# Performance work log

Measured on AMD Instinct MI355X. Metric: run time of the kernel, lower is better.

Reference implementation:

```python
import jax, jax.numpy as jnp
import numpy as np

EMBED = 768
NH = 12          # num_heads
NL = 3           # num_levels
NP = 4           # num_points
DV = 384         # value dim = embed_dim * deform_ratio(0.5)
DH = DV // NH    # per-head value dim = 32
B = 16
LQ = 1024        # (512/16)^2 ViT tokens
SHAPES = [(64, 64), (32, 32), (16, 16)]  # 1/8, 1/16, 1/32 pyramid of 512x512
LKV = sum(h * w for h, w in SHAPES)      # 5376
EPS = 1e-6


def layer_norm(x, w, b):
    mu = jnp.mean(x, axis=-1, keepdims=True)
    var = jnp.mean((x - mu) ** 2, axis=-1, keepdims=True)
    return (x - mu) / jnp.sqrt(var + EPS) * w + b


def bilinear_sample(v, loc, H, W):
    # v: (B, NH, H*W, DH); loc: (B, Lq, NH, P, 2) normalized in [0,1]
    # Matches torch grid_sample(align_corners=False, padding_mode='zeros').
    Bv, Lq = loc.shape[0], loc.shape[1]
    x = loc[..., 0] * W - 0.5
    y = loc[..., 1] * H - 0.5
    x0 = jnp.floor(x)
    y0 = jnp.floor(y)
    dx = x - x0
    dy = y - y0
    x0i = x0.astype(jnp.int32)
    y0i = y0.astype(jnp.int32)

    def gather(xi, yi):
        valid = (xi >= 0) & (xi < W) & (yi >= 0) & (yi < H)  # (B,Lq,NH,P)
        xc = jnp.clip(xi, 0, W - 1)
        yc = jnp.clip(yi, 0, H - 1)
        lin = (yc * W + xc).transpose(0, 2, 1, 3).reshape(Bv, NH, Lq * NP)
        g = jnp.take_along_axis(v, lin[..., None], axis=2)  # (B,NH,Lq*P,DH)
        g = g.reshape(Bv, NH, Lq, NP, DH).transpose(0, 2, 1, 3, 4)  # (B,Lq,NH,P,DH)
        return g * valid[..., None].astype(g.dtype)

    g00 = gather(x0i, y0i)
    g01 = gather(x0i + 1, y0i)
    g10 = gather(x0i, y0i + 1)
    g11 = gather(x0i + 1, y0i + 1)
    w00 = ((1 - dx) * (1 - dy))[..., None]
    w01 = (dx * (1 - dy))[..., None]
    w10 = ((1 - dx) * dy)[..., None]
    w11 = (dx * dy)[..., None]
    return g00 * w00 + g01 * w01 + g10 * w10 + g11 * w11


def ms_deform_attn_core(value, shapes_list, loc, aw):
    # value: (B,LKV,NH,DH); loc: (B,Lq,NH,NL,NP,2); aw: (B,Lq,NH,NL,NP)
    Bv, Lq = loc.shape[0], loc.shape[1]
    samples = []
    idx = 0
    for l, (H, W) in enumerate(shapes_list):
        v = value[:, idx:idx + H * W].transpose(0, 2, 1, 3)  # (B,NH,HW,DH)
        idx += H * W
        samples.append(bilinear_sample(v, loc[:, :, :, l], H, W))
    s = jnp.stack(samples, axis=3)  # (B,Lq,NH,NL,NP,DH)
    o = jnp.einsum('bqhlp,bqhlpd->bqhd', aw, s)
    return o.reshape(Bv, Lq, NH * DH)


def setup_inputs() -> dict:
    key = jax.random.key(0)
    ks = jax.random.split(key, 12)

    def n(k, shape, s=0.02):
        return jax.random.normal(k, shape, jnp.float32) * s

    return {
        'q': jax.random.normal(ks[0], (B, LQ, EMBED), jnp.float32),
        'reference_points': jax.random.uniform(ks[1], (B, LQ, NL, 2), jnp.float32),
        'kv': jax.random.normal(ks[2], (B, LKV, EMBED), jnp.float32),
        'spatial_shapes': jnp.asarray(SHAPES, jnp.int32),
        'level_start_index': jnp.asarray(
            np.cumsum([0] + [h * w for h, w in SHAPES])[:-1], jnp.int32),
        'ln1_w': jnp.ones(EMBED, jnp.float32),
        'ln1_b': jnp.zeros(EMBED, jnp.float32),
        'ln2_w': jnp.ones(EMBED, jnp.float32),
        'ln2_b': jnp.zeros(EMBED, jnp.float32),
        'gamma': n(ks[3], (EMBED,), 0.1),
        'w_off': n(ks[4], (EMBED, NH * NL * NP * 2)),
        'b_off': n(ks[5], (NH * NL * NP * 2,), 0.01),
        'w_aw': n(ks[6], (EMBED, NH * NL * NP)),
        'b_aw': jnp.zeros(NH * NL * NP, jnp.float32),
        'w_val': n(ks[7], (EMBED, DV)),
        'b_val': jnp.zeros(DV, jnp.float32),
        'w_out': n(ks[8], (DV, EMBED)),
        'b_out': jnp.zeros(EMBED, jnp.float32),
    }


def reference(q, reference_points, kv, spatial_shapes, level_start_index,
              ln1_w, ln1_b, ln2_w, ln2_b, gamma,
              w_off, b_off, w_aw, b_aw, w_val, b_val, w_out, b_out):
    shapes_list = [tuple(int(v) for v in r) for r in np.asarray(spatial_shapes)]
    Bq, Lq, _ = q.shape
    qn = layer_norm(q, ln1_w, ln1_b)
    kvn = layer_norm(kv, ln2_w, ln2_b)
    value = (kvn @ w_val + b_val).reshape(Bq, -1, NH, DH)
    off = (qn @ w_off + b_off).reshape(Bq, Lq, NH, NL, NP, 2)
    aw = (qn @ w_aw + b_aw).reshape(Bq, Lq, NH, NL * NP)
    aw = jax.nn.softmax(aw, axis=-1).reshape(Bq, Lq, NH, NL, NP)
    # offset normalizer is (W_l, H_l) per level
    wh = jnp.asarray([[w, h] for (h, w) in shapes_list], q.dtype)  # (NL,2)
    loc = reference_points[:, :, None, :, None, :] + off / wh[None, None, None, :, None, :]
    attn = ms_deform_attn_core(value, shapes_list, loc, aw)
    attn = attn @ w_out + b_out
    return q + gamma * attn
```

## Files before the change

kernel.cpp:

```cpp
#include <hip/hip_runtime.h>

#define DEV __device__ __forceinline__

typedef short bf16x8 __attribute__((ext_vector_type(8)));
typedef float f32x4 __attribute__((ext_vector_type(4)));

DEV short f2bf(float f) {
  union { float f; unsigned u; } un; un.f = f;
  unsigned r = un.u + 0x7FFFu + ((un.u >> 16) & 1u);
  return (short)(r >> 16);
}
DEV float bf2f(unsigned short s) {
  union { unsigned u; float f; } un;
  un.u = ((unsigned)s) << 16;
  return un.f;
}

DEV float blockReduceSum256(float v, volatile float* sbuf) {
  #pragma unroll
  for (int off = 32; off > 0; off >>= 1) v += __shfl_down(v, off, 64);
  const int wv = threadIdx.x >> 6, ln = threadIdx.x & 63;
  if (ln == 0) sbuf[wv] = v;
  __syncthreads();
  return sbuf[0] + sbuf[1] + sbuf[2] + sbuf[3];
}

__global__ __launch_bounds__(256) void pack_weights_kernel(
    const float* __restrict__ w_val, const float* __restrict__ w_off,
    const float* __restrict__ w_aw, const float* __restrict__ w_out,
    const float* __restrict__ b_off, const float* __restrict__ b_aw,
    short* __restrict__ wT_val, short* __restrict__ wT_offaw,
    short* __restrict__ wT_out, float* __restrict__ bias_cat) {
  int gid = blockIdx.x * 256 + threadIdx.x;
  const int S0 = 768 * 384, S1 = 768 * 288, S2 = 768 * 144, S3 = 384 * 768;
  const int S4 = 16 * 768, S5 = 448;
  if (gid < S0) { int k = gid / 384, n = gid % 384; wT_val[n * 768 + k] = f2bf(w_val[gid]); return; }
  gid -= S0;
  if (gid < S1) { int k = gid / 288, n = gid % 288; wT_offaw[n * 768 + k] = f2bf(w_off[gid]); return; }
  gid -= S1;
  if (gid < S2) { int k = gid / 144, n = gid % 144; wT_offaw[(288 + n) * 768 + k] = f2bf(w_aw[gid]); return; }
  gid -= S2;
  if (gid < S3) { int k = gid / 768, n = gid % 768; wT_out[n * 384 + k] = f2bf(w_out[gid]); return; }
  gid -= S3;
  if (gid < S4) { wT_offaw[432 * 768 + gid] = 0; return; }
  gid -= S4;
  if (gid < S5) { bias_cat[gid] = (gid < 288) ? b_off[gid] : (gid < 432 ? b_aw[gid - 288] : 0.f); }
}

__global__ __launch_bounds__(256) void ln_stats_kernel(const float* __restrict__ x,
                                                       float2* __restrict__ st) {
  const int row = blockIdx.x;
  const float* xr = x + (size_t)row * 768;
  const int t = threadIdx.x;
  float a0 = xr[t], a1 = xr[t + 256], a2 = xr[t + 512];
  __shared__ float sb1[4], sb2[4];
  float mu = blockReduceSum256(a0 + a1 + a2, sb1) * (1.f / 768.f);
  float d0 = a0 - mu, d1 = a1 - mu, d2 = a2 - mu;
  float var = blockReduceSum256(d0 * d0 + d1 * d1 + d2 * d2, sb2) * (1.f / 768.f);
  if (t == 0) st[row] = make_float2(mu, rsqrtf(var + 1e-6f));
}

template <int NT2, int AMODE, int EMODE>
__global__ __launch_bounds__(256, 2) void gemmw_kernel(
    const short* __restrict__ A, const float* __restrict__ Af,
    const float2* __restrict__ st, const float* __restrict__ lnw,
    const float* __restrict__ lnb, const short* __restrict__ Wt,
    const float* __restrict__ bias, const float* __restrict__ qres,
    const float* __restrict__ gamma, void* __restrict__ Cout,
    const int N, const int K) {
  constexpr int BN = NT2 * 64;
  __shared__ __align__(16) short As[64 * 40];
  __shared__ __align__(16) short Bs[BN * 40];
  const int tid = threadIdx.x;
  const int wave = tid >> 6, lane = tid & 63;
  const int sr = tid >> 2;
  const int sk = (tid & 3) * 8;
  const int n0 = blockIdx.x * BN;
  const int row0 = blockIdx.y * 64;
  const int lr = lane & 15, quad = lane >> 4;

  f32x4 acc[4][NT2];
  #pragma unroll
  for (int rt = 0; rt < 4; rt++)
    #pragma unroll
    for (int cb = 0; cb < NT2; cb++)
      #pragma unroll
      for (int j = 0; j < 4; j++) acc[rt][cb][j] = 0.f;

  const short* AsF = &As[lr * 40 + quad * 8];
  const short* BsF = &Bs[(wave * NT2 * 16 + lr) * 40 + quad * 8];

  float2 rowst = make_float2(0.f, 0.f);
  if (AMODE == 1) rowst = st[row0 + sr];

  for (int k0 = 0; k0 < K; k0 += 32) {
    if (AMODE == 0) {
      bf16x8 av = *(const bf16x8*)(A + (size_t)(row0 + sr) * K + k0 + sk);
      *(bf16x8*)(&As[sr * 40 + sk]) = av;
    } else {
      const float* p = Af + (size_t)(row0 + sr) * K + k0 + sk;
      float4 v0 = *(const float4*)p;
      float4 v1 = *(const float4*)(p + 4);
      const float* wp = lnw + k0 + sk;
      const float* bp = lnb + k0 + sk;
      float e[8] = {v0.x, v0.y, v0.z, v0.w, v1.x, v1.y, v1.z, v1.w};
      bf16x8 av;
      #pragma unroll
      for (int i = 0; i < 8; i++)
        av[i] = f2bf((e[i] - rowst.x) * rowst.y * wp[i] + bp[i]);
      *(bf16x8*)(&As[sr * 40 + sk]) = av;
    }
    #pragma unroll
    for (int i = tid; i < BN * 4; i += 256) {
      int n = i >> 2, kk = (i & 3) * 8;
      *(bf16x8*)(&Bs[n * 40 + kk]) =
          *(const bf16x8*)(Wt + (size_t)(n0 + n) * K + k0 + kk);
    }
    __syncthreads();
    bf16x8 af[4];
    #pragma unroll
    for (int rt = 0; rt < 4; rt++) af[rt] = *(const bf16x8*)(AsF + rt * 16 * 40);
    #pragma unroll
    for (int cb = 0; cb < NT2; cb++) {
      bf16x8 bf = *(const bf16x8*)(BsF + cb * 16 * 40);
      #pragma unroll
      for (int rt = 0; rt < 4; rt++)
        acc[rt][cb] = __builtin_amdgcn_mfma_f32_16x16x32_bf16(af[rt], bf, acc[rt][cb], 0, 0, 0);
    }
    __syncthreads();
  }

  #pragma unroll
  for (int cb = 0; cb < NT2; cb++) {
    const int n = n0 + wave * NT2 * 16 + cb * 16 + lr;
    const float bs = bias[n];
    const float gm = (EMODE == 2) ? gamma[n] : 0.f;
    #pragma unroll
    for (int rt = 0; rt < 4; rt++) {
      #pragma unroll
      for (int i = 0; i < 4; i++) {
        const int m = row0 + rt * 16 + quad * 4 + i;
        float v = acc[rt][cb][i] + bs;
        if (EMODE == 0) {
          ((short*)Cout)[(size_t)m * N + n] = f2bf(v);
        } else if (EMODE == 1) {
          ((float*)Cout)[(size_t)m * N + n] = v;
        } else {
          ((float*)Cout)[(size_t)m * N + n] =
              qres[(size_t)m * N + n] + gm * v;
        }
      }
    }
  }
}

__global__ __launch_bounds__(384) void sampler_kernel(
    const float* __restrict__ offaw,
    const float* __restrict__ refp,
    const short* __restrict__ value,
    short* __restrict__ o) {
  const int tid = threadIdx.x;
  const int qi = tid / 96, t = tid % 96;
  const int head = t >> 3, ln4 = t & 7;
  const int bq = blockIdx.x * 4 + qi;
  __shared__ __align__(16) float s[4][440];
  __shared__ float sref[4][6];
  const float* row = offaw + (size_t)bq * 448;
  #pragma unroll
  for (int i = t; i < 108; i += 96)
    *(float4*)&s[qi][i * 4] = *(const float4*)&row[i * 4];
  if (t < 6) sref[qi][t] = refp[(size_t)bq * 6 + t];
  __syncthreads();

  const float* awp = &s[qi][288 + head * 12];
  float mx = awp[0];
  #pragma unroll
  for (int j = 1; j < 12; j++) mx = fmaxf(mx, awp[j]);
  float wgt[12];
  float ssum = 0.f;
  #pragma unroll
  for (int j = 0; j < 12; j++) { float e = __expf(awp[j] - mx); wgt[j] = e; ssum += e; }
  const float inv = 1.f / ssum;

  const int b = bq >> 10;
  const unsigned short* vb =
      (const unsigned short*)value + (size_t)b * 5376 * 384 + head * 32 + ln4 * 4;
  float4 acc = make_float4(0.f, 0.f, 0.f, 0.f);
  const int HW[3] = {64, 32, 16};
  const int starts[3] = {0, 4096, 5120};
  #pragma unroll
  for (int l = 0; l < 3; l++) {
    const int Wi = HW[l];
    const float Wf = (float)Wi;
    const float rx = sref[qi][l * 2], ry = sref[qi][l * 2 + 1];
    const unsigned short* base = vb + (size_t)starts[l] * 384;
    #pragma unroll
    for (int p = 0; p < 4; p++) {
      const int oi = ((head * 3 + l) * 4 + p) * 2;
      float x = fmaf(rx, Wf, s[qi][oi] - 0.5f);
      float y = fmaf(ry, Wf, s[qi][oi + 1] - 0.5f);
      float xf = floorf(x), yf = floorf(y);
      float dx = x - xf, dy = y - yf;
      int x0 = (int)xf, y0 = (int)yf;
      int x1 = x0 + 1, y1 = y0 + 1;
      int x0c = min(max(x0, 0), Wi - 1), x1c = min(max(x1, 0), Wi - 1);
      int y0c = min(max(y0, 0), Wi - 1), y1c = min(max(y1, 0), Wi - 1);
      float wx0 = (x0 >= 0 && x0 < Wi) ? (1.f - dx) : 0.f;
      float wx1 = (x1 < Wi && x1 >= 0) ? dx : 0.f;
      float wy0 = (y0 >= 0 && y0 < Wi) ? (1.f - dy) : 0.f;
      float wy1 = (y1 < Wi && y1 >= 0) ? dy : 0.f;
      const ushort4 u00 = *(const ushort4*)(base + (size_t)(y0c * Wi + x0c) * 384);
      const ushort4 u01 = *(const ushort4*)(base + (size_t)(y0c * Wi + x1c) * 384);
      const ushort4 u10 = *(const ushort4*)(base + (size_t)(y1c * Wi + x0c) * 384);
      const ushort4 u11 = *(const ushort4*)(base + (size_t)(y1c * Wi + x1c) * 384);
      const float w00 = wx0 * wy0, w01 = wx1 * wy0, w10 = wx0 * wy1, w11 = wx1 * wy1;
      const float g = wgt[l * 4 + p];
      acc.x += g * (w00 * bf2f(u00.x) + w01 * bf2f(u01.x) + w10 * bf2f(u10.x) + w11 * bf2f(u11.x));
      acc.y += g * (w00 * bf2f(u00.y) + w01 * bf2f(u01.y) + w10 * bf2f(u10.y) + w11 * bf2f(u11.y));
      acc.z += g * (w00 * bf2f(u00.z) + w01 * bf2f(u01.z) + w10 * bf2f(u10.z) + w11 * bf2f(u11.z));
      acc.w += g * (w00 * bf2f(u00.w) + w01 * bf2f(u01.w) + w10 * bf2f(u10.w) + w11 * bf2f(u11.w));
    }
  }
  ushort4 out;
  out.x = (unsigned short)f2bf(acc.x * inv);
  out.y = (unsigned short)f2bf(acc.y * inv);
  out.z = (unsigned short)f2bf(acc.z * inv);
  out.w = (unsigned short)f2bf(acc.w * inv);
  *(ushort4*)((unsigned short*)o + (size_t)bq * 384 + head * 32 + ln4 * 4) = out;
}

extern "C" void kernel_launch(void* const* d_in, const int* in_sizes, int n_in,
                              void* d_out, int out_size, void* d_ws, size_t ws_size,
                              hipStream_t stream) {
  (void)in_sizes; (void)n_in; (void)out_size; (void)ws_size;
  const float* q     = (const float*)d_in[0];
  const float* refp  = (const float*)d_in[1];
  const float* kv    = (const float*)d_in[2];
  const float* ln1w  = (const float*)d_in[5];
  const float* ln1b  = (const float*)d_in[6];
  const float* ln2w  = (const float*)d_in[7];
  const float* ln2b  = (const float*)d_in[8];
  const float* gamma = (const float*)d_in[9];
  const float* w_off = (const float*)d_in[10];
  const float* b_off = (const float*)d_in[11];
  const float* w_aw  = (const float*)d_in[12];
  const float* b_aw  = (const float*)d_in[13];
  const float* w_val = (const float*)d_in[14];
  const float* b_val = (const float*)d_in[15];
  const float* w_out = (const float*)d_in[16];
  const float* b_out = (const float*)d_in[17];
  float* out = (float*)d_out;

  char* wsp = (char*)d_ws;
  size_t cur = 0;
  auto alloc = [&](size_t bytes) -> void* {
    cur = (cur + 255) & ~(size_t)255;
    void* p = wsp + cur;
    cur += bytes;
    return p;
  };
  short*  wT_val   = (short*)alloc((size_t)384 * 768 * 2);
  short*  wT_offaw = (short*)alloc((size_t)448 * 768 * 2);
  short*  wT_out   = (short*)alloc((size_t)768 * 384 * 2);
  float*  bias_cat = (float*)alloc((size_t)448 * 4);
  float2* st_kv    = (float2*)alloc((size_t)86016 * 8);
  float2* st_q     = (float2*)alloc((size_t)16384 * 8);
  short*  value    = (short*)alloc((size_t)86016 * 384 * 2);
  float*  offaw    = (float*)alloc((size_t)16384 * 448 * 4);
  short*  obuf     = (short*)alloc((size_t)16384 * 384 * 2);

  pack_weights_kernel<<<3651, 256, 0, stream>>>(w_val, w_off, w_aw, w_out, b_off,
                                                b_aw, wT_val, wT_offaw, wT_out,
                                                bias_cat);
  ln_stats_kernel<<<86016, 256, 0, stream>>>(kv, st_kv);
  ln_stats_kernel<<<16384, 256, 0, stream>>>(q, st_q);
  gemmw_kernel<6, 1, 0><<<dim3(1, 1344), 256, 0, stream>>>(
      nullptr, kv, st_kv, ln2w, ln2b, wT_val, b_val, nullptr, nullptr, value,
      384, 768);
  gemmw_kernel<7, 1, 1><<<dim3(1, 256), 256, 0, stream>>>(
      nullptr, q, st_q, ln1w, ln1b, wT_offaw, bias_cat, nullptr, nullptr, offaw,
      448, 768);
  sampler_kernel<<<4096, 384, 0, stream>>>(offaw, refp, value, obuf);
  gemmw_kernel<6, 0, 2><<<dim3(2, 256), 256, 0, stream>>>(
      obuf, nullptr, nullptr, nullptr, nullptr, wT_out, b_out, q, gamma, out,
      768, 384);
}
```

Baseline: 742.6 us.

## Materialize LayerNorm output in bf16 and use 128x128 LDS-direct GEMM tiles

LayerNorm is now applied in its own pass that writes normalized bf16 activations, so the GEMMs no longer normalize fp32 inputs while loading. The value projection and the output projection move to a new 128x128-tile GEMM that loads global memory straight into LDS through global_load_lds, with an XOR-swizzled LDS layout and a 2x2 wave grid. The intent is more data reuse per tile and cheaper A-operand loads. In exchange, the normalized kv (about 132 MB bf16) and q are written to and read back from memory. The new kernel also has no double buffering.

```diff
diff --git a/kernel.cpp b/kernel.cpp
--- a/kernel.cpp
+++ b/kernel.cpp
@@ -4,6 +4,9 @@
 
 typedef short bf16x8 __attribute__((ext_vector_type(8)));
 typedef float f32x4 __attribute__((ext_vector_type(4)));
+typedef unsigned int u32;
+typedef __attribute__((address_space(1))) const u32* gas_ptr;
+typedef __attribute__((address_space(3))) u32* las_ptr;
 
 DEV short f2bf(float f) {
   union { float f; unsigned u; } un; un.f = f;
@@ -14,6 +17,9 @@
   union { unsigned u; float f; } un;
   un.u = ((unsigned)s) << 16;
   return un.f;
+}
+DEV void gload16(const short* g, short* l) {
+  __builtin_amdgcn_global_load_lds((gas_ptr)g, (las_ptr)l, 16, 0, 0);
 }
 
 DEV float blockReduceSum256(float v, volatile float* sbuf) {
@@ -47,8 +53,9 @@
   if (gid < S5) { bias_cat[gid] = (gid < 288) ? b_off[gid] : (gid < 432 ? b_aw[gid - 288] : 0.f); }
 }
 
-__global__ __launch_bounds__(256) void ln_stats_kernel(const float* __restrict__ x,
-                                                       float2* __restrict__ st) {
+__global__ __launch_bounds__(256) void ln_norm_kernel(
+    const float* __restrict__ x, const float* __restrict__ w,
+    const float* __restrict__ b, short* __restrict__ y) {
   const int row = blockIdx.x;
   const float* xr = x + (size_t)row * 768;
   const int t = threadIdx.x;
@@ -57,16 +64,104 @@
   float mu = blockReduceSum256(a0 + a1 + a2, sb1) * (1.f / 768.f);
   float d0 = a0 - mu, d1 = a1 - mu, d2 = a2 - mu;
   float var = blockReduceSum256(d0 * d0 + d1 * d1 + d2 * d2, sb2) * (1.f / 768.f);
-  if (t == 0) st[row] = make_float2(mu, rsqrtf(var + 1e-6f));
-}
-
-template <int NT2, int AMODE, int EMODE>
-__global__ __launch_bounds__(256, 2) void gemmw_kernel(
-    const short* __restrict__ A, const float* __restrict__ Af,
-    const float2* __restrict__ st, const float* __restrict__ lnw,
-    const float* __restrict__ lnb, const short* __restrict__ Wt,
+  const float rs = rsqrtf(var + 1e-6f);
+  short* yr = y + (size_t)row * 768;
+  yr[t]       = f2bf(d0 * rs * w[t]       + b[t]);
+  yr[t + 256] = f2bf(d1 * rs * w[t + 256] + b[t + 256]);
+  yr[t + 512] = f2bf(d2 * rs * w[t + 512] + b[t + 512]);
+}
+
+template <int EMODE>
+__global__ __launch_bounds__(256, 3) void gemm128_kernel(
+    const short* __restrict__ A, const short* __restrict__ Wt,
     const float* __restrict__ bias, const float* __restrict__ qres,
     const float* __restrict__ gamma, void* __restrict__ Cout,
+    const int N, const int K) {
+  __shared__ __align__(16) short As[128 * 32];
+  __shared__ __align__(16) short Bs[128 * 32];
+  const int tid = threadIdx.x;
+  const int wave = tid >> 6, lane = tid & 63;
+  const int n0 = blockIdx.x * 128, row0 = blockIdx.y * 128;
+  const int lr = lane & 15, quad = lane >> 4;
+  const int wm = wave >> 1, wn = wave & 1;
+
+  const short* gA[2]; const short* gB[2];
+  #pragma unroll
+  for (int rnd = 0; rnd < 2; rnd++) {
+    int G = rnd * 256 + wave * 64 + lane;
+    int line = G >> 3, pos = G & 7, x = pos ^ (line & 7);
+    int r = line * 2 + (x >> 2), qk = (x & 3) * 8;
+    gA[rnd] = A + (size_t)(row0 + r) * K + qk;
+    gB[rnd] = Wt + (size_t)(n0 + r) * K + qk;
+  }
+  short* ldsA[2] = {&As[(wave * 64) * 8], &As[(256 + wave * 64) * 8]};
+  short* ldsB[2] = {&Bs[(wave * 64) * 8], &Bs[(256 + wave * 64) * 8]};
+
+  const short* aF[4]; const short* bF[4];
+  #pragma unroll
+  for (int t4 = 0; t4 < 4; t4++) {
+    int r = wm * 64 + t4 * 16 + lr;
+    int line = r >> 1, pos = ((r & 1) * 4 + quad) ^ (line & 7);
+    aF[t4] = &As[(line * 8 + pos) * 8];
+    int rb = wn * 64 + t4 * 16 + lr;
+    int lineb = rb >> 1, posb = ((rb & 1) * 4 + quad) ^ (lineb & 7);
+    bF[t4] = &Bs[(lineb * 8 + posb) * 8];
+  }
+
+  f32x4 acc[4][4];
+  #pragma unroll
+  for (int i = 0; i < 4; i++)
+    #pragma unroll
+    for (int j = 0; j < 4; j++)
+      #pragma unroll
+      for (int e = 0; e < 4; e++) acc[i][j][e] = 0.f;
+
+  for (int k0 = 0; k0 < K; k0 += 32) {
+    gload16(gA[0], ldsA[0]);
+    gload16(gA[1], ldsA[1]);
+    gload16(gB[0], ldsB[0]);
+    gload16(gB[1], ldsB[1]);
+    gA[0] += 32; gA[1] += 32; gB[0] += 32; gB[1] += 32;
+    __syncthreads();
+    bf16x8 av[4], bv[4];
+    #pragma unroll
+    for (int t4 = 0; t4 < 4; t4++) {
+      av[t4] = *(const bf16x8*)aF[t4];
+      bv[t4] = *(const bf16x8*)bF[t4];
+    }
+    #pragma unroll
+    for (int ct = 0; ct < 4; ct++)
+      #pragma unroll
+      for (int rt = 0; rt < 4; rt++)
+        acc[rt][ct] = __builtin_amdgcn_mfma_f32_16x16x32_bf16(av[rt], bv[ct], acc[rt][ct], 0, 0, 0);
+    __syncthreads();
+  }
+
+  #pragma unroll
+  for (int ct = 0; ct < 4; ct++) {
+    const int n = n0 + wn * 64 + ct * 16 + lr;
+    const float bs = bias[n];
+    const float gm = (EMODE == 2) ? gamma[n] : 0.f;
+    #pragma unroll
+    for (int rt = 0; rt < 4; rt++) {
+      #pragma unroll
+      for (int i = 0; i < 4; i++) {
+        const int m = row0 + wm * 64 + rt * 16 + quad * 4 + i;
+        float v = acc[rt][ct][i] + bs;
+        if (EMODE == 0) {
+          ((short*)Cout)[(size_t)m * N + n] = f2bf(v);
+        } else {
+          ((float*)Cout)[(size_t)m * N + n] = qres[(size_t)m * N + n] + gm * v;
+        }
+      }
+    }
+  }
+}
+
+template <int NT2>
+__global__ __launch_bounds__(256, 2) void gemmw_kernel(
+    const short* __restrict__ A, const short* __restrict__ Wt,
+    const float* __restrict__ bias, float* __restrict__ Cout,
     const int N, const int K) {
   constexpr int BN = NT2 * 64;
   __shared__ __align__(16) short As[64 * 40];
@@ -90,26 +185,9 @@
   const short* AsF = &As[lr * 40 + quad * 8];
   const short* BsF = &Bs[(wave * NT2 * 16 + lr) * 40 + quad * 8];
 
-  float2 rowst = make_float2(0.f, 0.f);
-  if (AMODE == 1) rowst = st[row0 + sr];
-
   for (int k0 = 0; k0 < K; k0 += 32) {
-    if (AMODE == 0) {
-      bf16x8 av = *(const bf16x8*)(A + (size_t)(row0 + sr) * K + k0 + sk);
-      *(bf16x8*)(&As[sr * 40 + sk]) = av;
-    } else {
-      const float* p = Af + (size_t)(row0 + sr) * K + k0 + sk;
-      float4 v0 = *(const float4*)p;
-      float4 v1 = *(const float4*)(p + 4);
-      const float* wp = lnw + k0 + sk;
-      const float* bp = lnb + k0 + sk;
-      float e[8] = {v0.x, v0.y, v0.z, v0.w, v1.x, v1.y, v1.z, v1.w};
-      bf16x8 av;
-      #pragma unroll
-      for (int i = 0; i < 8; i++)
-        av[i] = f2bf((e[i] - rowst.x) * rowst.y * wp[i] + bp[i]);
-      *(bf16x8*)(&As[sr * 40 + sk]) = av;
-    }
+    bf16x8 av = *(const bf16x8*)(A + (size_t)(row0 + sr) * K + k0 + sk);
+    *(bf16x8*)(&As[sr * 40 + sk]) = av;
     #pragma unroll
     for (int i = tid; i < BN * 4; i += 256) {
       int n = i >> 2, kk = (i & 3) * 8;
@@ -122,10 +200,10 @@
     for (int rt = 0; rt < 4; rt++) af[rt] = *(const bf16x8*)(AsF + rt * 16 * 40);
     #pragma unroll
     for (int cb = 0; cb < NT2; cb++) {
-      bf16x8 bf = *(const bf16x8*)(BsF + cb * 16 * 40);
+      bf16x8 bfv = *(const bf16x8*)(BsF + cb * 16 * 40);
       #pragma unroll
       for (int rt = 0; rt < 4; rt++)
-        acc[rt][cb] = __builtin_amdgcn_mfma_f32_16x16x32_bf16(af[rt], bf, acc[rt][cb], 0, 0, 0);
+        acc[rt][cb] = __builtin_amdgcn_mfma_f32_16x16x32_bf16(af[rt], bfv, acc[rt][cb], 0, 0, 0);
     }
     __syncthreads();
   }
@@ -134,21 +212,12 @@
   for (int cb = 0; cb < NT2; cb++) {
     const int n = n0 + wave * NT2 * 16 + cb * 16 + lr;
     const float bs = bias[n];
-    const float gm = (EMODE == 2) ? gamma[n] : 0.f;
     #pragma unroll
     for (int rt = 0; rt < 4; rt++) {
       #pragma unroll
       for (int i = 0; i < 4; i++) {
         const int m = row0 + rt * 16 + quad * 4 + i;
-        float v = acc[rt][cb][i] + bs;
-        if (EMODE == 0) {
-          ((short*)Cout)[(size_t)m * N + n] = f2bf(v);
-        } else if (EMODE == 1) {
-          ((float*)Cout)[(size_t)m * N + n] = v;
-        } else {
-          ((float*)Cout)[(size_t)m * N + n] =
-              qres[(size_t)m * N + n] + gm * v;
-        }
+        Cout[(size_t)m * N + n] = acc[rt][cb][i] + bs;
       }
     }
   }
@@ -221,12 +290,12 @@
       acc.w += g * (w00 * bf2f(u00.w) + w01 * bf2f(u01.w) + w10 * bf2f(u10.w) + w11 * bf2f(u11.w));
     }
   }
-  ushort4 out;
-  out.x = (unsigned short)f2bf(acc.x * inv);
-  out.y = (unsigned short)f2bf(acc.y * inv);
-  out.z = (unsigned short)f2bf(acc.z * inv);
-  out.w = (unsigned short)f2bf(acc.w * inv);
-  *(ushort4*)((unsigned short*)o + (size_t)bq * 384 + head * 32 + ln4 * 4) = out;
+  ushort4 outv;
+  outv.x = (unsigned short)f2bf(acc.x * inv);
+  outv.y = (unsigned short)f2bf(acc.y * inv);
+  outv.z = (unsigned short)f2bf(acc.z * inv);
+  outv.w = (unsigned short)f2bf(acc.w * inv);
+  *(ushort4*)((unsigned short*)o + (size_t)bq * 384 + head * 32 + ln4 * 4) = outv;
 }
 
 extern "C" void kernel_launch(void* const* d_in, const int* in_sizes, int n_in,
@@ -263,8 +332,8 @@
   short*  wT_offaw = (short*)alloc((size_t)448 * 768 * 2);
   short*  wT_out   = (short*)alloc((size_t)768 * 384 * 2);
   float*  bias_cat = (float*)alloc((size_t)448 * 4);
-  float2* st_kv    = (float2*)alloc((size_t)86016 * 8);
-  float2* st_q     = (float2*)alloc((size_t)16384 * 8);
+  short*  kvn      = (short*)alloc((size_t)86016 * 768 * 2);
+  short*  qn       = (short*)alloc((size_t)16384 * 768 * 2);
   short*  value    = (short*)alloc((size_t)86016 * 384 * 2);
   float*  offaw    = (float*)alloc((size_t)16384 * 448 * 4);
   short*  obuf     = (short*)alloc((size_t)16384 * 384 * 2);
@@ -272,16 +341,13 @@
   pack_weights_kernel<<<3651, 256, 0, stream>>>(w_val, w_off, w_aw, w_out, b_off,
                                                 b_aw, wT_val, wT_offaw, wT_out,
                                                 bias_cat);
-  ln_stats_kernel<<<86016, 256, 0, stream>>>(kv, st_kv);
-  ln_stats_kernel<<<16384, 256, 0, stream>>>(q, st_q);
-  gemmw_kernel<6, 1, 0><<<dim3(1, 1344), 256, 0, stream>>>(
-      nullptr, kv, st_kv, ln2w, ln2b, wT_val, b_val, nullptr, nullptr, value,
-      384, 768);
-  gemmw_kernel<7, 1, 1><<<dim3(1, 256), 256, 0, stream>>>(
-      nullptr, q, st_q, ln1w, ln1b, wT_offaw, bias_cat, nullptr, nullptr, offaw,
-      448, 768);
+  ln_norm_kernel<<<86016, 256, 0, stream>>>(kv, ln2w, ln2b, kvn);
+  ln_norm_kernel<<<16384, 256, 0, stream>>>(q, ln1w, ln1b, qn);
+  gemm128_kernel<0><<<dim3(3, 672), 256, 0, stream>>>(
+      kvn, wT_val, b_val, nullptr, nullptr, value, 384, 768);
+  gemmw_kernel<7><<<dim3(1, 256), 256, 0, stream>>>(
+      qn, wT_offaw, bias_cat, offaw, 448, 768);
   sampler_kernel<<<4096, 384, 0, stream>>>(offaw, refp, value, obuf);
-  gemmw_kernel<6, 0, 2><<<dim3(2, 256), 256, 0, stream>>>(
-      obuf, nullptr, nullptr, nullptr, nullptr, wT_out, b_out, q, gamma, out,
-      768, 384);
-}
+  gemm128_kernel<2><<<dim3(6, 128), 256, 0, stream>>>(
+      obuf, wT_out, b_out, q, gamma, out, 768, 384);
+}
```

Result: no change. 732.4 us (-1.4%).
